# Kernel optimization log

Measured on AMD Instinct MI355X. Metric: run time of the kernel, lower is better.

Reference implementation:

```python
import jax, jax.numpy as jnp
import numpy as np

B, C, H, W = 4, 3, 1024, 1024
RADII = (8, 16, 32, 64)
EPS = 1e-5  # BatchNorm2d default eps


def _box_sum(x, r, s):
    # depthwise all-ones conv (kernel r, stride s, VALID padding) == summed box
    return jax.lax.reduce_window(x, 0.0, jax.lax.add, (1, 1, r, r), (1, 1, s, s), 'VALID')


def _axis_interp_ac(x, n_out, axis):
    # bilinear (align_corners=True) interpolation along one axis
    n_in = x.shape[axis]
    pos = jnp.arange(n_out, dtype=x.dtype) * ((n_in - 1) / max(n_out - 1, 1))
    i0 = jnp.clip(jnp.floor(pos).astype(jnp.int32), 0, n_in - 2)
    w = pos - i0.astype(x.dtype)
    a = jnp.take(x, i0, axis=axis)
    b = jnp.take(x, i0 + 1, axis=axis)
    shape = [1] * x.ndim
    shape[axis] = n_out
    w = w.reshape(shape)
    return a * (1 - w) + b * w


def _resize_ac(x, oh, ow):
    x = _axis_interp_ac(x, oh, 2)
    x = _axis_interp_ac(x, ow, 3)
    return x


def _bn(x, g, b, rm, rv):
    inv = g / jnp.sqrt(rv + EPS)
    return x * inv[None, :, None, None] + (b - rm * inv)[None, :, None, None]


def _forward(guide, src, w1, g1, b1, rm1, rv1, w2, g2, b2, rm2, rv2, w3):
    Hg, Wg = guide.shape[2], guide.shape[3]
    gg = guide * guide
    gs = guide * src
    ones = jnp.ones((1, guide.shape[1], Hg, Wg), guide.dtype)
    stats = []
    for r in RADII:
        s = r // 2
        N = _box_sum(ones, r, s)
        mx = _box_sum(guide, r, s) / N
        my = _box_sum(src, r, s) / N
        cov = _box_sum(gs, r, s) / N - mx * my
        var = _box_sum(gg, r, s) / N - mx * mx
        stats.append((mx, my, cov, var))
    mx1, my1, cov1, var1 = stats[0]
    oh, ow = cov1.shape[2], cov1.shape[3]
    feats = [cov1, var1]
    for (_, _, cov, var) in stats[1:]:
        feats.append(_resize_ac(cov, oh, ow))
        feats.append(_resize_ac(var, oh, ow))
    x = jnp.concatenate(feats, axis=1)  # [B,24,oh,ow]
    x = jax.nn.relu(_bn(jnp.einsum('oc,bchw->bohw', w1, x), g1, b1, rm1, rv1))
    x = jax.nn.relu(_bn(jnp.einsum('oc,bchw->bohw', w2, x), g2, b2, rm2, rv2))
    A = jnp.einsum('oc,bchw->bohw', w3, x)  # [B,3,oh,ow]
    bb = my1 - A * mx1
    mean_A = _resize_ac(A, Hg, Wg)
    mean_b = _resize_ac(bb, Hg, Wg)
    return mean_A * guide + mean_b


def setup_inputs() -> dict:
    key = jax.random.key(0)
    ks = jax.random.split(key, 5)
    f32 = jnp.float32
    return {
        'guide': jax.random.normal(ks[0], (B, C, H, W), f32),
        'src': jax.random.normal(ks[1], (B, C, H, W), f32),
        'w1': jax.random.normal(ks[2], (48, 24), f32) * 0.05,
        'g1': jnp.ones((48,), f32), 'b1': jnp.zeros((48,), f32),
        'rm1': jnp.zeros((48,), f32), 'rv1': jnp.ones((48,), f32),
        'w2': jax.random.normal(ks[3], (48, 48), f32) * 0.05,
        'g2': jnp.ones((48,), f32), 'b2': jnp.zeros((48,), f32),
        'rm2': jnp.zeros((48,), f32), 'rv2': jnp.ones((48,), f32),
        'w3': jax.random.normal(ks[4], (3, 48), f32) * 0.05,
    }


def reference(guide, src, w1, g1, b1, rm1, rv1, w2, g2, b2, rm2, rv2, w3):
    return _forward(guide, src, w1, g1, b1, rm1, rv1, w2, g2, b2, rm2, rv2, w3)
```

## Files before the change

### kernel.cpp

```cpp
#include <hip/hip_runtime.h>

typedef float v2f __attribute__((ext_vector_type(2)));

#define HH 1024
#define WW 1024
#define NB 4
#define NC 3
#define BC 12
#define N1 255
#define N2 127
#define N3 63
#define N4 31
#define EPS 1e-5f

constexpr size_t S8_OFF  = 0;
constexpr size_t S8_SZ   = 4ull * BC * N1 * N1;
constexpr size_t CV16_OFF = S8_OFF + S8_SZ;
constexpr size_t CV16_SZ  = 2ull * BC * N2 * N2;
constexpr size_t CV32_OFF = CV16_OFF + CV16_SZ;
constexpr size_t CV32_SZ  = 2ull * BC * N3 * N3;
constexpr size_t CV64_OFF = CV32_OFF + CV32_SZ;
constexpr size_t CV64_SZ  = 2ull * BC * N4 * N4;
constexpr size_t A_OFF    = CV64_OFF + CV64_SZ;
constexpr size_t A_SZ     = (size_t)NB * NC * N1 * N1;
constexpr size_t BB_OFF   = A_OFF + A_SZ;

__global__ __launch_bounds__(256) void base_kernel(
    const float* __restrict__ guide, const float* __restrict__ src,
    float* __restrict__ S8)
{
    __shared__ float smem[8][WW];

    int b  = blockIdx.x % 128;
    int bc = blockIdx.x / 128;
    int t  = threadIdx.x;

    const float* gbase = guide + (size_t)bc * HH * WW + 4 * t;
    const float* sbase = src   + (size_t)bc * HH * WW + 4 * t;

    float pg[3][4], ps[3][4], pgg[3][4], pgs[3][4];
#pragma unroll
    for (int grp = 0; grp < 3; ++grp)
#pragma unroll
        for (int k = 0; k < 4; ++k) {
            pg[grp][k] = 0.f; ps[grp][k] = 0.f;
            pgg[grp][k] = 0.f; pgs[grp][k] = 0.f;
        }

#pragma unroll
    for (int grp = 0; grp < 3; ++grp) {
#pragma unroll
        for (int r = 0; r < 4; ++r) {
            int row = 8 * b + 4 * grp + r;
            if (row < HH) {
                float4 g4 = *(const float4*)(gbase + (size_t)row * WW);
                float4 s4 = *(const float4*)(sbase + (size_t)row * WW);
                float ge[4] = {g4.x, g4.y, g4.z, g4.w};
                float se[4] = {s4.x, s4.y, s4.z, s4.w};
#pragma unroll
                for (int k = 0; k < 4; ++k) {
                    pg[grp][k]  += ge[k];
                    ps[grp][k]  += se[k];
                    pgg[grp][k] += ge[k] * ge[k];
                    pgs[grp][k] += ge[k] * se[k];
                }
            }
        }
    }

#pragma unroll
    for (int k = 0; k < 4; ++k) {
        int c = 4 * t + k;
        smem[0][c] = pg[0][k]  + pg[1][k];
        smem[1][c] = ps[0][k]  + ps[1][k];
        smem[2][c] = pgg[0][k] + pgg[1][k];
        smem[3][c] = pgs[0][k] + pgs[1][k];
        smem[4][c] = pg[1][k]  + pg[2][k];
        smem[5][c] = ps[1][k]  + ps[2][k];
        smem[6][c] = pgg[1][k] + pgg[2][k];
        smem[7][c] = pgs[1][k] + pgs[2][k];
    }
    __syncthreads();

    if (t < N1) {
        size_t qs   = (size_t)BC * N1 * N1;
        size_t base = (size_t)bc * N1 * N1;
#pragma unroll
        for (int rsel = 0; rsel < 2; ++rsel) {
            int i = 2 * b + rsel;
            if (i < N1) {
#pragma unroll
                for (int q = 0; q < 4; ++q) {
                    const float* arr = smem[4 * rsel + q];
                    float4 a4 = *(const float4*)(arr + 4 * t);
                    float4 b4 = *(const float4*)(arr + 4 * t + 4);
                    float v = (a4.x + a4.y) + (a4.z + a4.w) +
                              (b4.x + b4.y) + (b4.z + b4.w);
                    S8[(size_t)q * qs + base + (size_t)i * N1 + t] = v;
                }
            }
        }
    }
}

__global__ __launch_bounds__(256) void pyr_all(
    const float* __restrict__ S8, float* __restrict__ CV16,
    float* __restrict__ CV32, float* __restrict__ CV64)
{
    const int n2t = BC * N2 * N2, n3t = BC * N3 * N3, n4t = BC * N4 * N4;
    int idx = blockIdx.x * 256 + threadIdx.x;

    float* CV; int nout, cnt; float invN; int rem;
    if (idx < n2t)              { CV = CV16; nout = N2; cnt = 2; invN = 1.f / 256.f;  rem = idx; }
    else if (idx < n2t + n3t)   { CV = CV32; nout = N3; cnt = 4; invN = 1.f / 1024.f; rem = idx - n2t; }
    else if (idx < n2t + n3t + n4t) { CV = CV64; nout = N4; cnt = 8; invN = 1.f / 4096.f; rem = idx - n2t - n3t; }
    else return;

    int j  = rem % nout;
    int tt = rem / nout;
    int i  = tt % nout;
    int bc = tt / nout;

    size_t qs = (size_t)BC * N1 * N1;
    const float* P = S8 + (size_t)bc * N1 * N1;
    int p0 = cnt * i, q0 = cnt * j;

    float s0 = 0.f, s1 = 0.f, s2 = 0.f, s3 = 0.f;
    for (int ky = 0; ky < cnt; ++ky) {
        size_t roff = (size_t)(p0 + 2 * ky) * N1 + q0;
        for (int kx = 0; kx < cnt; ++kx) {
            size_t o = roff + 2 * kx;
            s0 += P[0 * qs + o];
            s1 += P[1 * qs + o];
            s2 += P[2 * qs + o];
            s3 += P[3 * qs + o];
        }
    }

    size_t sOut = (size_t)BC * nout * nout;
    size_t o    = (size_t)bc * nout * nout + (size_t)i * nout + j;
    float mx = s0 * invN, my = s1 * invN;
    CV[o]        = s3 * invN - mx * my;
    CV[sOut + o] = s2 * invN - mx * mx;
}

__global__ __launch_bounds__(128) void mlp_kernel(
    const float* __restrict__ S8,
    const float* __restrict__ CV16, const float* __restrict__ CV32,
    const float* __restrict__ CV64,
    const float* __restrict__ w1, const float* __restrict__ g1,
    const float* __restrict__ b1, const float* __restrict__ rm1,
    const float* __restrict__ rv1,
    const float* __restrict__ w2, const float* __restrict__ g2,
    const float* __restrict__ b2, const float* __restrict__ rm2,
    const float* __restrict__ rv2,
    const float* __restrict__ w3,
    float* __restrict__ A, float* __restrict__ Bb)
{
    __shared__ float sw1[48 * 24], sw2[48 * 48], sw3[3 * 48];
    __shared__ float inv1[48], bia1[48], inv2[48], bia2[48];
    int t = threadIdx.x;
    for (int k = t; k < 48 * 24; k += 128) sw1[k] = w1[k];
    for (int k = t; k < 48 * 48; k += 128) sw2[k] = w2[k];
    for (int k = t; k < 3 * 48; k += 128) sw3[k] = w3[k];
    if (t < 48) {
        float iv = g1[t] * rsqrtf(rv1[t] + EPS);
        inv1[t] = iv; bia1[t] = b1[t] - rm1[t] * iv;
        float iv2 = g2[t] * rsqrtf(rv2[t] + EPS);
        inv2[t] = iv2; bia2[t] = b2[t] - rm2[t] * iv2;
    }
    __syncthreads();

    int idx = blockIdx.x * 128 + t;
    if (idx >= NB * N1 * N1) return;
    int ox = idx % N1;
    int r  = idx / N1;
    int oy = r % N1;
    int b  = r / N1;

    float feats[24], mx1[3], my1[3];

    size_t s8q = (size_t)BC * N1 * N1;
#pragma unroll
    for (int c = 0; c < 3; ++c) {
        size_t o = (size_t)(b * 3 + c) * N1 * N1 + (size_t)oy * N1 + ox;
        float sg = S8[o], ss = S8[s8q + o], sgg = S8[2 * s8q + o], sgs = S8[3 * s8q + o];
        float mx = sg * (1.f / 64.f), my = ss * (1.f / 64.f);
        mx1[c] = mx; my1[c] = my;
        feats[c]     = sgs * (1.f / 64.f) - mx * my;
        feats[3 + c] = sgg * (1.f / 64.f) - mx * mx;
    }

    const float* CVs[3] = {CV16, CV32, CV64};
    const int nins[3]   = {N2, N3, N4};
    const float scales[3] = {(float)(126.0 / 254.0), (float)(62.0 / 254.0),
                             (float)(30.0 / 254.0)};
#pragma unroll
    for (int l = 0; l < 3; ++l) {
        const float* CV = CVs[l];
        int nin = nins[l];
        float sc = scales[l];
        float py = (float)oy * sc;
        int   i0 = min(max((int)floorf(py), 0), nin - 2);
        float wy = py - (float)i0;
        float px = (float)ox * sc;
        int   j0 = min(max((int)floorf(px), 0), nin - 2);
        float wx = px - (float)j0;
        size_t cvq = (size_t)BC * nin * nin;
        int fo = 6 + 6 * l;
#pragma unroll
        for (int c = 0; c < 3; ++c) {
            size_t bix = (size_t)(b * 3 + c) * nin * nin;
            size_t o00 = bix + (size_t)i0 * nin + j0;
            float c00 = CV[o00], c01 = CV[o00 + 1];
            float c10 = CV[o00 + nin], c11 = CV[o00 + nin + 1];
            feats[fo + c] = (c00 * (1.f - wy) + c10 * wy) * (1.f - wx) +
                            (c01 * (1.f - wy) + c11 * wy) * wx;
            float v00 = CV[cvq + o00], v01 = CV[cvq + o00 + 1];
            float v10 = CV[cvq + o00 + nin], v11 = CV[cvq + o00 + nin + 1];
            feats[fo + 3 + c] = (v00 * (1.f - wy) + v10 * wy) * (1.f - wx) +
                                (v01 * (1.f - wy) + v11 * wy) * wx;
        }
    }

    v2f f2[12];
#pragma unroll
    for (int k = 0; k < 12; ++k) { f2[k][0] = feats[2 * k]; f2[k][1] = feats[2 * k + 1]; }

    v2f h1v[24];
#pragma unroll
    for (int o = 0; o < 48; ++o) {
        const v2f* wrow = (const v2f*)(&sw1[o * 24]);
        v2f acc = {0.f, 0.f};
#pragma unroll
        for (int c = 0; c < 12; ++c) acc += wrow[c] * f2[c];
        float v = fmaxf((acc[0] + acc[1]) * inv1[o] + bia1[o], 0.f);
        h1v[o >> 1][o & 1] = v;
    }
    v2f h2v[24];
#pragma unroll
    for (int o = 0; o < 48; ++o) {
        const v2f* wrow = (const v2f*)(&sw2[o * 48]);
        v2f acc = {0.f, 0.f};
#pragma unroll
        for (int c = 0; c < 24; ++c) acc += wrow[c] * h1v[c];
        float v = fmaxf((acc[0] + acc[1]) * inv2[o] + bia2[o], 0.f);
        h2v[o >> 1][o & 1] = v;
    }
#pragma unroll
    for (int c = 0; c < 3; ++c) {
        const v2f* wrow = (const v2f*)(&sw3[c * 48]);
        v2f acc = {0.f, 0.f};
#pragma unroll
        for (int k = 0; k < 24; ++k) acc += wrow[k] * h2v[k];
        float a = acc[0] + acc[1];
        size_t o = (size_t)(b * 3 + c) * N1 * N1 + (size_t)oy * N1 + ox;
        A[o]  = a;
        Bb[o] = my1[c] - a * mx1[c];
    }
}

__global__ __launch_bounds__(256) void final_kernel(
    const float* __restrict__ guide, const float* __restrict__ A,
    const float* __restrict__ Bb, float* __restrict__ out)
{
    __shared__ float aH[N1 + 1], bH[N1 + 1];
    int blk = blockIdx.x;
    int bc  = blk / HH;
    int h   = blk % HH;

    const float scale = (float)(254.0 / 1023.0);
    float py = (float)h * scale;
    int   i0 = min(max((int)floorf(py), 0), N1 - 2);
    float wy = py - (float)i0;

    int t = threadIdx.x;
    if (t < N1) {
        size_t base = (size_t)bc * N1 * N1 + (size_t)i0 * N1 + t;
        aH[t] = A[base] * (1.f - wy) + A[base + N1] * wy;
        bH[t] = Bb[base] * (1.f - wy) + Bb[base + N1] * wy;
    }
    __syncthreads();

    const float* gp = guide + (size_t)bc * HH * WW + (size_t)h * WW;
    float*       op = out   + (size_t)bc * HH * WW + (size_t)h * WW;

    float4 g4 = *(const float4*)(gp + 4 * t);
    float ge[4] = {g4.x, g4.y, g4.z, g4.w};
    float oe[4];
#pragma unroll
    for (int k = 0; k < 4; ++k) {
        int w = 4 * t + k;
        float px = (float)w * scale;
        int   j0 = min(max((int)floorf(px), 0), N1 - 2);
        float wx = px - (float)j0;
        float a   = aH[j0] * (1.f - wx) + aH[j0 + 1] * wx;
        float bbv = bH[j0] * (1.f - wx) + bH[j0 + 1] * wx;
        oe[k] = a * ge[k] + bbv;
    }
    float4 o4; o4.x = oe[0]; o4.y = oe[1]; o4.z = oe[2]; o4.w = oe[3];
    *(float4*)(op + 4 * t) = o4;
}

extern "C" void kernel_launch(void* const* d_in, const int* in_sizes, int n_in,
                              void* d_out, int out_size, void* d_ws, size_t ws_size,
                              hipStream_t stream)
{
    const float* guide = (const float*)d_in[0];
    const float* src   = (const float*)d_in[1];
    const float* w1    = (const float*)d_in[2];
    const float* g1    = (const float*)d_in[3];
    const float* b1    = (const float*)d_in[4];
    const float* rm1   = (const float*)d_in[5];
    const float* rv1   = (const float*)d_in[6];
    const float* w2    = (const float*)d_in[7];
    const float* g2    = (const float*)d_in[8];
    const float* b2    = (const float*)d_in[9];
    const float* rm2   = (const float*)d_in[10];
    const float* rv2   = (const float*)d_in[11];
    const float* w3    = (const float*)d_in[12];
    float*       out   = (float*)d_out;

    float* ws   = (float*)d_ws;
    float* S8   = ws + S8_OFF;
    float* CV16 = ws + CV16_OFF;
    float* CV32 = ws + CV32_OFF;
    float* CV64 = ws + CV64_OFF;
    float* Abuf = ws + A_OFF;
    float* Bbuf = ws + BB_OFF;

    base_kernel<<<BC * 128, 256, 0, stream>>>(guide, src, S8);

    {
        int total = BC * (N2 * N2 + N3 * N3 + N4 * N4);
        pyr_all<<<(total + 255) / 256, 256, 0, stream>>>(S8, CV16, CV32, CV64);
    }

    {
        int total = NB * N1 * N1;
        mlp_kernel<<<(total + 127) / 128, 128, 0, stream>>>(
            S8, CV16, CV32, CV64, w1, g1, b1, rm1, rv1, w2, g2, b2, rm2, rv2, w3,
            Abuf, Bbuf);
    }

    final_kernel<<<BC * HH, 256, 0, stream>>>(guide, Abuf, Bbuf, out);
}
```

Baseline: 255.4 us.

## Interleave intermediate stats and A/b buffers; process two pixels per MLP thread

Intermediate buffers change from planar to interleaved layouts: S8 stores its four statistics as one float4, the CV pyramids store cov/var as v2f, and A/b are packed as v2f. Each gather then becomes a single wide load instead of several scattered scalar ones. The MLP kernel now handles two pixels per thread, packed into v2f lanes, so every weight loaded from shared memory is reused across both pixels; block size rises to 256. The cost is higher register pressure in the MLP (48-element v2f arrays), which may lower occupancy or cause spills.

After: 238.0 us. 1.07x faster.

```diff
diff --git a/kernel.cpp b/kernel.cpp
--- a/kernel.cpp
+++ b/kernel.cpp
@@ -12,22 +12,22 @@
 #define N3 63
 #define N4 31
 #define EPS 1e-5f
-
-constexpr size_t S8_OFF  = 0;
-constexpr size_t S8_SZ   = 4ull * BC * N1 * N1;
+#define NPIX (NB * N1 * N1)
+#define NPAIR (NPIX / 2)
+
+constexpr size_t S8_OFF = 0;
+constexpr size_t S8_SZ  = 4ull * BC * N1 * N1;
 constexpr size_t CV16_OFF = S8_OFF + S8_SZ;
 constexpr size_t CV16_SZ  = 2ull * BC * N2 * N2;
 constexpr size_t CV32_OFF = CV16_OFF + CV16_SZ;
 constexpr size_t CV32_SZ  = 2ull * BC * N3 * N3;
 constexpr size_t CV64_OFF = CV32_OFF + CV32_SZ;
 constexpr size_t CV64_SZ  = 2ull * BC * N4 * N4;
-constexpr size_t A_OFF    = CV64_OFF + CV64_SZ;
-constexpr size_t A_SZ     = (size_t)NB * NC * N1 * N1;
-constexpr size_t BB_OFF   = A_OFF + A_SZ;
+constexpr size_t AB_OFF = CV64_OFF + CV64_SZ;
 
 __global__ __launch_bounds__(256) void base_kernel(
     const float* __restrict__ guide, const float* __restrict__ src,
-    float* __restrict__ S8)
+    float4* __restrict__ S8q)
 {
     __shared__ float smem[8][WW];
 
@@ -83,34 +83,35 @@
     __syncthreads();
 
     if (t < N1) {
-        size_t qs   = (size_t)BC * N1 * N1;
-        size_t base = (size_t)bc * N1 * N1;
+        size_t plane = (size_t)bc * N1 * N1;
 #pragma unroll
         for (int rsel = 0; rsel < 2; ++rsel) {
             int i = 2 * b + rsel;
             if (i < N1) {
+                float qv[4];
 #pragma unroll
                 for (int q = 0; q < 4; ++q) {
                     const float* arr = smem[4 * rsel + q];
                     float4 a4 = *(const float4*)(arr + 4 * t);
                     float4 b4 = *(const float4*)(arr + 4 * t + 4);
-                    float v = (a4.x + a4.y) + (a4.z + a4.w) +
-                              (b4.x + b4.y) + (b4.z + b4.w);
-                    S8[(size_t)q * qs + base + (size_t)i * N1 + t] = v;
+                    qv[q] = (a4.x + a4.y) + (a4.z + a4.w) +
+                            (b4.x + b4.y) + (b4.z + b4.w);
                 }
+                float4 o4; o4.x = qv[0]; o4.y = qv[1]; o4.z = qv[2]; o4.w = qv[3];
+                S8q[plane + (size_t)i * N1 + t] = o4;
             }
         }
     }
 }
 
 __global__ __launch_bounds__(256) void pyr_all(
-    const float* __restrict__ S8, float* __restrict__ CV16,
-    float* __restrict__ CV32, float* __restrict__ CV64)
+    const float4* __restrict__ S8q, v2f* __restrict__ CV16,
+    v2f* __restrict__ CV32, v2f* __restrict__ CV64)
 {
     const int n2t = BC * N2 * N2, n3t = BC * N3 * N3, n4t = BC * N4 * N4;
     int idx = blockIdx.x * 256 + threadIdx.x;
 
-    float* CV; int nout, cnt; float invN; int rem;
+    v2f* CV; int nout, cnt; float invN; int rem;
     if (idx < n2t)              { CV = CV16; nout = N2; cnt = 2; invN = 1.f / 256.f;  rem = idx; }
     else if (idx < n2t + n3t)   { CV = CV32; nout = N3; cnt = 4; invN = 1.f / 1024.f; rem = idx - n2t; }
     else if (idx < n2t + n3t + n4t) { CV = CV64; nout = N4; cnt = 8; invN = 1.f / 4096.f; rem = idx - n2t - n3t; }
@@ -121,33 +122,28 @@
     int i  = tt % nout;
     int bc = tt / nout;
 
-    size_t qs = (size_t)BC * N1 * N1;
-    const float* P = S8 + (size_t)bc * N1 * N1;
+    const float4* P = S8q + (size_t)bc * N1 * N1;
     int p0 = cnt * i, q0 = cnt * j;
 
     float s0 = 0.f, s1 = 0.f, s2 = 0.f, s3 = 0.f;
     for (int ky = 0; ky < cnt; ++ky) {
         size_t roff = (size_t)(p0 + 2 * ky) * N1 + q0;
         for (int kx = 0; kx < cnt; ++kx) {
-            size_t o = roff + 2 * kx;
-            s0 += P[0 * qs + o];
-            s1 += P[1 * qs + o];
-            s2 += P[2 * qs + o];
-            s3 += P[3 * qs + o];
-        }
-    }
-
-    size_t sOut = (size_t)BC * nout * nout;
-    size_t o    = (size_t)bc * nout * nout + (size_t)i * nout + j;
+            float4 q4 = P[roff + 2 * kx];
+            s0 += q4.x; s1 += q4.y; s2 += q4.z; s3 += q4.w;
+        }
+    }
+
+    size_t o = (size_t)bc * nout * nout + (size_t)i * nout + j;
     float mx = s0 * invN, my = s1 * invN;
-    CV[o]        = s3 * invN - mx * my;
-    CV[sOut + o] = s2 * invN - mx * mx;
-}
-
-__global__ __launch_bounds__(128) void mlp_kernel(
-    const float* __restrict__ S8,
-    const float* __restrict__ CV16, const float* __restrict__ CV32,
-    const float* __restrict__ CV64,
+    v2f cv; cv[0] = s3 * invN - mx * my; cv[1] = s2 * invN - mx * mx;
+    CV[o] = cv;
+}
+
+__global__ __launch_bounds__(256) void mlp_kernel(
+    const float4* __restrict__ S8q,
+    const v2f* __restrict__ CV16, const v2f* __restrict__ CV32,
+    const v2f* __restrict__ CV64,
     const float* __restrict__ w1, const float* __restrict__ g1,
     const float* __restrict__ b1, const float* __restrict__ rm1,
     const float* __restrict__ rv1,
@@ -155,116 +151,144 @@
     const float* __restrict__ b2, const float* __restrict__ rm2,
     const float* __restrict__ rv2,
     const float* __restrict__ w3,
-    float* __restrict__ A, float* __restrict__ Bb)
-{
-    __shared__ float sw1[48 * 24], sw2[48 * 48], sw3[3 * 48];
+    v2f* __restrict__ AB)
+{
+    __shared__ float4 sw1q[288], sw2q[576], sw3q[36];
     __shared__ float inv1[48], bia1[48], inv2[48], bia2[48];
     int t = threadIdx.x;
-    for (int k = t; k < 48 * 24; k += 128) sw1[k] = w1[k];
-    for (int k = t; k < 48 * 48; k += 128) sw2[k] = w2[k];
-    for (int k = t; k < 3 * 48; k += 128) sw3[k] = w3[k];
-    if (t < 48) {
-        float iv = g1[t] * rsqrtf(rv1[t] + EPS);
-        inv1[t] = iv; bia1[t] = b1[t] - rm1[t] * iv;
-        float iv2 = g2[t] * rsqrtf(rv2[t] + EPS);
-        inv2[t] = iv2; bia2[t] = b2[t] - rm2[t] * iv2;
+    {
+        const float4* w1q = (const float4*)w1;
+        const float4* w2q = (const float4*)w2;
+        const float4* w3q = (const float4*)w3;
+        for (int k = t; k < 288; k += 256) sw1q[k] = w1q[k];
+        for (int k = t; k < 576; k += 256) sw2q[k] = w2q[k];
+        if (t < 36) sw3q[t] = w3q[t];
+        if (t < 48) {
+            float iv = g1[t] * rsqrtf(rv1[t] + EPS);
+            inv1[t] = iv; bia1[t] = b1[t] - rm1[t] * iv;
+            float iv2 = g2[t] * rsqrtf(rv2[t] + EPS);
+            inv2[t] = iv2; bia2[t] = b2[t] - rm2[t] * iv2;
+        }
     }
     __syncthreads();
 
-    int idx = blockIdx.x * 128 + t;
-    if (idx >= NB * N1 * N1) return;
-    int ox = idx % N1;
-    int r  = idx / N1;
-    int oy = r % N1;
-    int b  = r / N1;
-
-    float feats[24], mx1[3], my1[3];
-
-    size_t s8q = (size_t)BC * N1 * N1;
-#pragma unroll
-    for (int c = 0; c < 3; ++c) {
-        size_t o = (size_t)(b * 3 + c) * N1 * N1 + (size_t)oy * N1 + ox;
-        float sg = S8[o], ss = S8[s8q + o], sgg = S8[2 * s8q + o], sgs = S8[3 * s8q + o];
-        float mx = sg * (1.f / 64.f), my = ss * (1.f / 64.f);
-        mx1[c] = mx; my1[c] = my;
-        feats[c]     = sgs * (1.f / 64.f) - mx * my;
-        feats[3 + c] = sgg * (1.f / 64.f) - mx * mx;
-    }
-
-    const float* CVs[3] = {CV16, CV32, CV64};
-    const int nins[3]   = {N2, N3, N4};
+    int gid = blockIdx.x * 256 + t;
+    if (gid >= NPAIR) return;
+
+    float fA[24], fB[24], mxs[2][3], mys[2][3];
+    int bs[2], inpl[2];
+
     const float scales[3] = {(float)(126.0 / 254.0), (float)(62.0 / 254.0),
                              (float)(30.0 / 254.0)};
-#pragma unroll
-    for (int l = 0; l < 3; ++l) {
-        const float* CV = CVs[l];
-        int nin = nins[l];
-        float sc = scales[l];
-        float py = (float)oy * sc;
-        int   i0 = min(max((int)floorf(py), 0), nin - 2);
-        float wy = py - (float)i0;
-        float px = (float)ox * sc;
-        int   j0 = min(max((int)floorf(px), 0), nin - 2);
-        float wx = px - (float)j0;
-        size_t cvq = (size_t)BC * nin * nin;
-        int fo = 6 + 6 * l;
+
+#pragma unroll
+    for (int s = 0; s < 2; ++s) {
+        int pidx = 2 * gid + s;
+        int ox = pidx % N1;
+        int r  = pidx / N1;
+        int oy = r % N1;
+        int b  = r / N1;
+        bs[s] = b; inpl[s] = oy * N1 + ox;
+        float* f = s ? fB : fA;
+
 #pragma unroll
         for (int c = 0; c < 3; ++c) {
-            size_t bix = (size_t)(b * 3 + c) * nin * nin;
-            size_t o00 = bix + (size_t)i0 * nin + j0;
-            float c00 = CV[o00], c01 = CV[o00 + 1];
-            float c10 = CV[o00 + nin], c11 = CV[o00 + nin + 1];
-            feats[fo + c] = (c00 * (1.f - wy) + c10 * wy) * (1.f - wx) +
-                            (c01 * (1.f - wy) + c11 * wy) * wx;
-            float v00 = CV[cvq + o00], v01 = CV[cvq + o00 + 1];
-            float v10 = CV[cvq + o00 + nin], v11 = CV[cvq + o00 + nin + 1];
-            feats[fo + 3 + c] = (v00 * (1.f - wy) + v10 * wy) * (1.f - wx) +
-                                (v01 * (1.f - wy) + v11 * wy) * wx;
-        }
-    }
-
-    v2f f2[12];
-#pragma unroll
-    for (int k = 0; k < 12; ++k) { f2[k][0] = feats[2 * k]; f2[k][1] = feats[2 * k + 1]; }
-
-    v2f h1v[24];
+            float4 q4 = S8q[(size_t)(b * 3 + c) * N1 * N1 + (size_t)oy * N1 + ox];
+            float mx = q4.x * (1.f / 64.f), my = q4.y * (1.f / 64.f);
+            mxs[s][c] = mx; mys[s][c] = my;
+            f[c]     = q4.w * (1.f / 64.f) - mx * my;
+            f[3 + c] = q4.z * (1.f / 64.f) - mx * mx;
+        }
+
+        const v2f* CVs[3] = {CV16, CV32, CV64};
+        const int nins[3] = {N2, N3, N4};
+#pragma unroll
+        for (int l = 0; l < 3; ++l) {
+            const v2f* CV = CVs[l];
+            int nin = nins[l];
+            float sc = scales[l];
+            float py = (float)oy * sc;
+            int   i0 = min(max((int)floorf(py), 0), nin - 2);
+            float wy = py - (float)i0;
+            float px = (float)ox * sc;
+            int   j0 = min(max((int)floorf(px), 0), nin - 2);
+            float wx = px - (float)j0;
+            int fo = 6 + 6 * l;
+#pragma unroll
+            for (int c = 0; c < 3; ++c) {
+                size_t o00 = (size_t)(b * 3 + c) * nin * nin + (size_t)i0 * nin + j0;
+                v2f c00 = CV[o00], c01 = CV[o00 + 1];
+                v2f c10 = CV[o00 + nin], c11 = CV[o00 + nin + 1];
+                v2f res = (c00 * (1.f - wy) + c10 * wy) * (1.f - wx) +
+                          (c01 * (1.f - wy) + c11 * wy) * wx;
+                f[fo + c]     = res[0];
+                f[fo + 3 + c] = res[1];
+            }
+        }
+    }
+
+    v2f f2[24];
+#pragma unroll
+    for (int c = 0; c < 24; ++c) { f2[c][0] = fA[c]; f2[c][1] = fB[c]; }
+
+    v2f h1[48];
 #pragma unroll
     for (int o = 0; o < 48; ++o) {
-        const v2f* wrow = (const v2f*)(&sw1[o * 24]);
+        const float4* wr = &sw1q[o * 6];
         v2f acc = {0.f, 0.f};
 #pragma unroll
-        for (int c = 0; c < 12; ++c) acc += wrow[c] * f2[c];
-        float v = fmaxf((acc[0] + acc[1]) * inv1[o] + bia1[o], 0.f);
-        h1v[o >> 1][o & 1] = v;
-    }
-    v2f h2v[24];
+        for (int k = 0; k < 6; ++k) {
+            float4 wq = wr[k];
+            acc += (v2f){wq.x, wq.x} * f2[4 * k + 0];
+            acc += (v2f){wq.y, wq.y} * f2[4 * k + 1];
+            acc += (v2f){wq.z, wq.z} * f2[4 * k + 2];
+            acc += (v2f){wq.w, wq.w} * f2[4 * k + 3];
+        }
+        float iv = inv1[o], bb = bia1[o];
+        v2f h; h[0] = fmaxf(acc[0] * iv + bb, 0.f); h[1] = fmaxf(acc[1] * iv + bb, 0.f);
+        h1[o] = h;
+    }
+    v2f h2[48];
 #pragma unroll
     for (int o = 0; o < 48; ++o) {
-        const v2f* wrow = (const v2f*)(&sw2[o * 48]);
+        const float4* wr = &sw2q[o * 12];
         v2f acc = {0.f, 0.f};
 #pragma unroll
-        for (int c = 0; c < 24; ++c) acc += wrow[c] * h1v[c];
-        float v = fmaxf((acc[0] + acc[1]) * inv2[o] + bia2[o], 0.f);
-        h2v[o >> 1][o & 1] = v;
+        for (int k = 0; k < 12; ++k) {
+            float4 wq = wr[k];
+            acc += (v2f){wq.x, wq.x} * h1[4 * k + 0];
+            acc += (v2f){wq.y, wq.y} * h1[4 * k + 1];
+            acc += (v2f){wq.z, wq.z} * h1[4 * k + 2];
+            acc += (v2f){wq.w, wq.w} * h1[4 * k + 3];
+        }
+        float iv = inv2[o], bb = bia2[o];
+        v2f h; h[0] = fmaxf(acc[0] * iv + bb, 0.f); h[1] = fmaxf(acc[1] * iv + bb, 0.f);
+        h2[o] = h;
     }
 #pragma unroll
     for (int c = 0; c < 3; ++c) {
-        const v2f* wrow = (const v2f*)(&sw3[c * 48]);
+        const float4* wr = &sw3q[c * 12];
         v2f acc = {0.f, 0.f};
 #pragma unroll
-        for (int k = 0; k < 24; ++k) acc += wrow[k] * h2v[k];
-        float a = acc[0] + acc[1];
-        size_t o = (size_t)(b * 3 + c) * N1 * N1 + (size_t)oy * N1 + ox;
-        A[o]  = a;
-        Bb[o] = my1[c] - a * mx1[c];
+        for (int k = 0; k < 12; ++k) {
+            float4 wq = wr[k];
+            acc += (v2f){wq.x, wq.x} * h2[4 * k + 0];
+            acc += (v2f){wq.y, wq.y} * h2[4 * k + 1];
+            acc += (v2f){wq.z, wq.z} * h2[4 * k + 2];
+            acc += (v2f){wq.w, wq.w} * h2[4 * k + 3];
+        }
+        v2f outA; outA[0] = acc[0]; outA[1] = mys[0][c] - acc[0] * mxs[0][c];
+        v2f outB; outB[0] = acc[1]; outB[1] = mys[1][c] - acc[1] * mxs[1][c];
+        AB[(size_t)(bs[0] * 3 + c) * N1 * N1 + inpl[0]] = outA;
+        AB[(size_t)(bs[1] * 3 + c) * N1 * N1 + inpl[1]] = outB;
     }
 }
 
 __global__ __launch_bounds__(256) void final_kernel(
-    const float* __restrict__ guide, const float* __restrict__ A,
-    const float* __restrict__ Bb, float* __restrict__ out)
-{
-    __shared__ float aH[N1 + 1], bH[N1 + 1];
+    const float* __restrict__ guide, const v2f* __restrict__ AB,
+    float* __restrict__ out)
+{
+    __shared__ v2f abH[N1 + 1];
     int blk = blockIdx.x;
     int bc  = blk / HH;
     int h   = blk % HH;
@@ -277,8 +301,8 @@
     int t = threadIdx.x;
     if (t < N1) {
         size_t base = (size_t)bc * N1 * N1 + (size_t)i0 * N1 + t;
-        aH[t] = A[base] * (1.f - wy) + A[base + N1] * wy;
-        bH[t] = Bb[base] * (1.f - wy) + Bb[base + N1] * wy;
+        v2f p0 = AB[base], p1 = AB[base + N1];
+        abH[t] = p0 * (1.f - wy) + p1 * wy;
     }
     __syncthreads();
 
@@ -294,9 +318,8 @@
         float px = (float)w * scale;
         int   j0 = min(max((int)floorf(px), 0), N1 - 2);
         float wx = px - (float)j0;
-        float a   = aH[j0] * (1.f - wx) + aH[j0 + 1] * wx;
-        float bbv = bH[j0] * (1.f - wx) + bH[j0 + 1] * wx;
-        oe[k] = a * ge[k] + bbv;
+        v2f ab = abH[j0] * (1.f - wx) + abH[j0 + 1] * wx;
+        oe[k] = ab[0] * ge[k] + ab[1];
     }
     float4 o4; o4.x = oe[0]; o4.y = oe[1]; o4.z = oe[2]; o4.w = oe[3];
     *(float4*)(op + 4 * t) = o4;
@@ -321,27 +344,22 @@
     const float* w3    = (const float*)d_in[12];
     float*       out   = (float*)d_out;
 
-    float* ws   = (float*)d_ws;
-    float* S8   = ws + S8_OFF;
-    float* CV16 = ws + CV16_OFF;
-    float* CV32 = ws + CV32_OFF;
-    float* CV64 = ws + CV64_OFF;
-    float* Abuf = ws + A_OFF;
-    float* Bbuf = ws + BB_OFF;
-
-    base_kernel<<<BC * 128, 256, 0, stream>>>(guide, src, S8);
+    float* ws    = (float*)d_ws;
+    float4* S8q  = (float4*)(ws + S8_OFF);
+    v2f*   CV16  = (v2f*)(ws + CV16_OFF);
+    v2f*   CV32  = (v2f*)(ws + CV32_OFF);
+    v2f*   CV64  = (v2f*)(ws + CV64_OFF);
+    v2f*   AB    = (v2f*)(ws + AB_OFF);
+
+    base_kernel<<<BC * 128, 256, 0, stream>>>(guide, src, S8q);
 
     {
         int total = BC * (N2 * N2 + N3 * N3 + N4 * N4);
-        pyr_all<<<(total + 255) / 256, 256, 0, stream>>>(S8, CV16, CV32, CV64);
-    }
-
-    {
-        int total = NB * N1 * N1;
-        mlp_kernel<<<(total + 127) / 128, 128, 0, stream>>>(
-            S8, CV16, CV32, CV64, w1, g1, b1, rm1, rv1, w2, g2, b2, rm2, rv2, w3,
-            Abuf, Bbuf);
-    }
-
-    final_kernel<<<BC * HH, 256, 0, stream>>>(guide, Abuf, Bbuf, out);
-}
+        pyr_all<<<(total + 255) / 256, 256, 0, stream>>>(S8q, CV16, CV32, CV64);
+    }
+
+    mlp_kernel<<<(NPAIR + 255) / 256, 256, 0, stream>>>(
+        S8q, CV16, CV32, CV64, w1, g1, b1, rm1, rv1, w2, g2, b2, rm2, rv2, w3, AB);
+
+    final_kernel<<<BC * HH, 256, 0, stream>>>(guide, AB, out);
+}
```
